# Kernel optimization log

Measured on AMD Instinct MI355X. Metric: run time of the kernel, lower is better.

The kernel has to match this reference:

```python
import jax, jax.numpy as jnp
import numpy as np

N_NODES, N_EDGES, DIM = 50000, 800000, 128


def setup_inputs() -> dict:
    key = jax.random.key(0)
    ks = jax.random.split(key, 16)
    s = 1.0 / np.sqrt(DIM)
    inp = {
        "x": jax.random.normal(ks[0], (N_NODES, DIM), dtype=jnp.float32),
        "edge_index": jax.random.randint(ks[1], (2, N_EDGES), 0, N_NODES, dtype=jnp.int64),
    }
    # 3 GIN layers, each with a 2-layer MLP (Linear-ReLU-Linear)
    for i in range(3):
        inp[f"w1_{i}"] = jax.random.normal(ks[2 + 4 * i], (DIM, DIM), dtype=jnp.float32) * s
        inp[f"b1_{i}"] = jnp.zeros((DIM,), dtype=jnp.float32)
        inp[f"w2_{i}"] = jax.random.normal(ks[3 + 4 * i], (DIM, DIM), dtype=jnp.float32) * s
        inp[f"b2_{i}"] = jnp.zeros((DIM,), dtype=jnp.float32)
    inp["wh"] = jax.random.normal(ks[14], (DIM, DIM), dtype=jnp.float32) * s
    inp["bh"] = jnp.zeros((DIM,), dtype=jnp.float32)
    return inp


def _gin_layer(h, src, dst, w1, b1, w2, b2, residual):
    # message passing: gather x[src], scatter-add at dst (aggr='sum')
    neigh = jax.ops.segment_sum(h[src], dst, num_segments=h.shape[0])
    out = h + neigh  # (1 + eps) * x + neigh, eps = 0
    out = jnp.maximum(out @ w1 + b1, 0.0) @ w2 + b2  # MLP (dropout p=0)
    if residual:  # res_fc is Identity since in_dim == out_dim
        out = out + h
    return out


def reference(x, edge_index, w1_0, b1_0, w2_0, b2_0, w1_1, b1_1, w2_1, b2_1,
              w1_2, b1_2, w2_2, b2_2, wh, bh):
    src, dst = edge_index[0], edge_index[1]
    h = x
    h = _gin_layer(h, src, dst, w1_0, b1_0, w2_0, b2_0, residual=True)
    h = _gin_layer(h, src, dst, w1_1, b1_1, w2_1, b2_1, residual=True)
    # last layer: encoding=False -> no residual
    h = _gin_layer(h, src, dst, w1_2, b1_2, w2_2, b2_2, residual=False)
    # extra_output_fc head
    return h @ wh + bh
```

## Files before the change

kernel.cpp:

```cpp
#include <hip/hip_runtime.h>
#include <hip/hip_fp16.h>

#define N_NODES 50000
#define N_EDGES 800000
#define DIM 128
#define FEAT_ELEMS (N_NODES * DIM)
#define STRIDE 64
#define NB 391
#define BCAP 3072

typedef __attribute__((ext_vector_type(8))) _Float16 f16x8;
typedef __attribute__((ext_vector_type(4))) float f32x4;
typedef __attribute__((ext_vector_type(2))) float f32x2;

#define MFMA_F16 __builtin_amdgcn_mfma_f32_16x16x32_f16


__global__ __launch_bounds__(256) void prep_combo_kernel(
    const float* __restrict__ w0, const float* __restrict__ w1,
    const float* __restrict__ w2, const float* __restrict__ w3,
    const float* __restrict__ w4, const float* __restrict__ w5,
    const float* __restrict__ w6, __half* __restrict__ dst,
    const float* __restrict__ x, __half* __restrict__ hm,
    unsigned char* __restrict__ qm, int* __restrict__ gcnt) {
    const int b = blockIdx.x;
    if (b < 112) {
        const int wsel = b >> 4;
        const int chunk = b & 15;
        const float* W;
        switch (wsel) {
            case 0: W = w0; break;
            case 1: W = w1; break;
            case 2: W = w2; break;
            case 3: W = w3; break;
            case 4: W = w4; break;
            case 5: W = w5; break;
            default: W = w6; break;
        }
        __half* d = dst + (size_t)wsel * 16384;
        int idx = chunk * 1024 + threadIdx.x;
#pragma unroll
        for (int t = 0; t < 4; ++t, idx += 256) {
            int k = idx >> 7, n = idx & 127;
            int ks = k >> 5, q = (k >> 3) & 3, j = k & 7;
            int ct = n >> 4, c = n & 15;
            int lane = q * 16 + c;
            int base = ((ks * 8 + ct) * 64 + lane) * 8 + j;
            d[base] = __float2half(W[idx]);
        }
    } else if (b < 1136) {
        int i = (b - 112) * 256 + threadIdx.x;
        const int stride = 1024 * 256;
        const int n4 = FEAT_ELEMS / 4;
        for (; i < n4; i += stride) {
            float4 v = ((const float4*)x)[i];
            __half2 h0 = __floats2half2_rn(v.x, v.y);
            __half2 h1 = __floats2half2_rn(v.z, v.w);
            uint2 u;
            u.x = *(unsigned*)&h0;
            u.y = *(unsigned*)&h1;
            ((uint2*)hm)[i] = u;
            int p = __builtin_amdgcn_cvt_pk_fp8_f32(v.x, v.y, 0, false);
            p = __builtin_amdgcn_cvt_pk_fp8_f32(v.z, v.w, p, true);
            ((int*)qm)[i] = p;
        }
    } else {
        for (int i = threadIdx.x; i < NB; i += 256) gcnt[i] = 0;
    }
}


__global__ __launch_bounds__(256) void bucket_kernel(const int* __restrict__ ei,
                                                     int* __restrict__ gcnt,
                                                     long long* __restrict__ ebuf) {
    __shared__ int hist[NB];
    __shared__ int base[NB];
    __shared__ int sh_is64;
    const int tid = threadIdx.x;
    for (int i = tid; i < NB; i += 256) hist[i] = 0;
    if (tid == 0) {
        int o = 0;
        for (int i = 1; i < 64; i += 2) o |= ei[i];
        sh_is64 = (o == 0) ? 1 : 0;
    }
    __syncthreads();
    const int e0 = blockIdx.x * 2048;
    const int is64 = sh_is64;
    int sv[8], dv[8];
    int nl = 0;
#pragma unroll
    for (int k = 0; k < 8; ++k) {
        int e = e0 + k * 256 + tid;
        if (e < N_EDGES) {
            int s = is64 ? ei[2 * e] : ei[e];
            int d = is64 ? ei[2 * (N_EDGES + e)] : ei[N_EDGES + e];
            sv[nl] = s;
            dv[nl] = d;
            atomicAdd(&hist[d >> 7], 1);
            ++nl;
        }
    }
    __syncthreads();
    for (int i = tid; i < NB; i += 256) {
        int h = hist[i];
        base[i] = h ? atomicAdd(&gcnt[i], h) : 0;
    }
    __syncthreads();
    for (int i = tid; i < NB; i += 256) hist[i] = 0;
    __syncthreads();
    for (int k = 0; k < nl; ++k) {
        int b = dv[k] >> 7;
        int r = base[b] + atomicAdd(&hist[b], 1);
        if (r < BCAP)
            ebuf[(size_t)b * BCAP + r] = ((long long)sv[k] << 32) | (unsigned)dv[k];
    }
}


__global__ __launch_bounds__(256) void build_kernel(const int* __restrict__ gcnt,
                                                    const long long* __restrict__ ebuf,
                                                    int* __restrict__ cnt,
                                                    int* __restrict__ col_idx) {
    __shared__ int cur[128];
    const int b = blockIdx.x;
    const int tid = threadIdx.x;
    if (tid < 128) cur[tid] = 0;
    __syncthreads();
    int n = gcnt[b];
    if (n > BCAP) n = BCAP;
    const long long* eb = ebuf + (size_t)b * BCAP;
    for (int i = tid; i < n; i += 256) {
        long long p = eb[i];
        int d = (int)(p & 0xFFFFFFFFll);
        int s = (int)(p >> 32);
        int slot = atomicAdd(&cur[d & 127], 1);
        if (slot < STRIDE) col_idx[d * STRIDE + slot] = s;
    }
    __syncthreads();
    int node = b * 128 + tid;
    if (tid < 128 && node < N_NODES) {
        int c = cur[tid];
        cnt[node] = (c > STRIDE) ? STRIDE : c;
    }
}


__global__ __launch_bounds__(256) void agg_kernel(const __half* __restrict__ selfH,
                                                  const unsigned char* __restrict__ Qm,
                                                  const int* __restrict__ cnt,
                                                  const int* __restrict__ col_idx,
                                                  __half* __restrict__ Tm) {
    const int hw = (blockIdx.x * 256 + threadIdx.x) >> 4;
    const int l = threadIdx.x & 15;
    const int d0 = l * 8;

    float acc[8];
    {
        uint4 sv = *(const uint4*)(selfH + (size_t)hw * DIM + d0);
        const __half2* sp = (const __half2*)&sv;
        float2 s0 = __half22float2(sp[0]), s1 = __half22float2(sp[1]);
        float2 s2 = __half22float2(sp[2]), s3 = __half22float2(sp[3]);
        acc[0] = s0.x; acc[1] = s0.y; acc[2] = s1.x; acc[3] = s1.y;
        acc[4] = s2.x; acc[5] = s2.y; acc[6] = s3.x; acc[7] = s3.y;
    }
    int d = cnt[hw];
    if (d > STRIDE) d = STRIDE;
    const int* ci = col_idx + hw * STRIDE;

#define ACCQ(U)                                                             \
    {                                                                       \
        f32x2 g0 = __builtin_amdgcn_cvt_pk_f32_fp8((int)(U).x, false);      \
        f32x2 g1 = __builtin_amdgcn_cvt_pk_f32_fp8((int)(U).x, true);       \
        f32x2 g2 = __builtin_amdgcn_cvt_pk_f32_fp8((int)(U).y, false);      \
        f32x2 g3 = __builtin_amdgcn_cvt_pk_f32_fp8((int)(U).y, true);       \
        acc[0] += g0.x; acc[1] += g0.y; acc[2] += g1.x; acc[3] += g1.y;     \
        acc[4] += g2.x; acc[5] += g2.y; acc[6] += g3.x; acc[7] += g3.y;     \
    }
    int j = 0;
    for (; j + 8 <= d; j += 8) {
        int s[8];
#pragma unroll
        for (int k = 0; k < 8; ++k) s[k] = ci[j + k];
        uint2 u[8];
#pragma unroll
        for (int k = 0; k < 8; ++k) u[k] = *(const uint2*)(Qm + (size_t)s[k] * DIM + d0);
#pragma unroll
        for (int k = 0; k < 8; ++k) ACCQ(u[k])
    }
    for (; j + 2 <= d; j += 2) {
        int s0 = ci[j], s1 = ci[j + 1];
        uint2 u0 = *(const uint2*)(Qm + (size_t)s0 * DIM + d0);
        uint2 u1 = *(const uint2*)(Qm + (size_t)s1 * DIM + d0);
        ACCQ(u0)
        ACCQ(u1)
    }
    if (j < d) {
        int s = ci[j];
        uint2 u = *(const uint2*)(Qm + (size_t)s * DIM + d0);
        ACCQ(u)
    }
#undef ACCQ

    uint4 o;
    __half2* op = (__half2*)&o;
    op[0] = __floats2half2_rn(acc[0], acc[1]);
    op[1] = __floats2half2_rn(acc[2], acc[3]);
    op[2] = __floats2half2_rn(acc[4], acc[5]);
    op[3] = __floats2half2_rn(acc[6], acc[7]);
    *(uint4*)(Tm + (size_t)hw * DIM + d0) = o;
}


template <bool RES, bool WQ>
__global__ __launch_bounds__(256, 4) void mlp_kernel(
    const __half* __restrict__ T,
    const __half* __restrict__ W1f,
    const __half* __restrict__ W2f,
    const float* __restrict__ b1,
    const float* __restrict__ b2,
    const __half* __restrict__ resH,
    __half* __restrict__ Hout,
    unsigned char* __restrict__ Qout) {
    __shared__ __align__(16) __half ul[4][2048];
    const int tid = threadIdx.x;
    const int lane = tid & 63;
    const int wid = tid >> 6;
    const int c = lane & 15;
    const int q = lane >> 4;
    const int R = (blockIdx.x * 4 + wid) * 16;
    if (R >= N_NODES) return;

    f16x8 a[4];
#pragma unroll
    for (int ks = 0; ks < 4; ++ks)
        a[ks] = *(const f16x8*)(T + (size_t)(R + c) * DIM + ks * 32 + q * 8);

    f32x4 acc1[8];
#pragma unroll
    for (int ct = 0; ct < 8; ++ct) acc1[ct] = (f32x4){0.f, 0.f, 0.f, 0.f};
#pragma unroll
    for (int ks = 0; ks < 4; ++ks) {
#pragma unroll
        for (int ct = 0; ct < 8; ++ct) {
            f16x8 b = *(const f16x8*)(W1f + (ks * 8 + ct) * 512 + lane * 8);
            acc1[ct] = MFMA_F16(a[ks], b, acc1[ct], 0, 0, 0);
        }
    }

#pragma unroll
    for (int ct = 0; ct < 8; ++ct) {
        const int col = ct * 16 + c;
        const float bv = b1[col];
#pragma unroll
        for (int rr = 0; rr < 4; ++rr) {
            const int rl = q * 4 + rr;
            ul[wid][rl * 128 + (col ^ ((rl & 7) << 3))] =
                __float2half(fmaxf(acc1[ct][rr] + bv, 0.f));
        }
    }

    f32x4 acc2[8];
#pragma unroll
    for (int ct = 0; ct < 8; ++ct) acc2[ct] = (f32x4){0.f, 0.f, 0.f, 0.f};
#pragma unroll
    for (int ks = 0; ks < 4; ++ks) {
        f16x8 ua = *(const f16x8*)&ul[wid][c * 128 + ((ks * 32 + q * 8) ^ ((c & 7) << 3))];
#pragma unroll
        for (int ct = 0; ct < 8; ++ct) {
            f16x8 b = *(const f16x8*)(W2f + (ks * 8 + ct) * 512 + lane * 8);
            acc2[ct] = MFMA_F16(ua, b, acc2[ct], 0, 0, 0);
        }
    }

#pragma unroll
    for (int ct = 0; ct < 8; ++ct) {
        const int col = ct * 16 + c;
        const float bv = b2[col];
#pragma unroll
        for (int rr = 0; rr < 4; ++rr) {
            const int rl = q * 4 + rr;
            ul[wid][rl * 128 + (col ^ (q << 4))] = __float2half(acc2[ct][rr] + bv);
        }
    }

    const int row2 = lane >> 2;
    const int cb = (lane & 3) * 8;
    const size_t grow = (size_t)(R + row2);
#pragma unroll
    for (int k = 0; k < 4; ++k) {
        const int c0 = cb + k * 32;
        uint4 hv = *(uint4*)&ul[wid][row2 * 128 + (c0 ^ ((row2 >> 2) << 4))];
        const __half2* hp = (const __half2*)&hv;
        float2 t0 = __half22float2(hp[0]), t1 = __half22float2(hp[1]);
        float2 t2 = __half22float2(hp[2]), t3 = __half22float2(hp[3]);
        float f0 = t0.x, f1 = t0.y, f2 = t1.x, f3 = t1.y;
        float f4 = t2.x, f5 = t2.y, f6 = t3.x, f7 = t3.y;
        if (RES) {
            uint4 rv = *(const uint4*)(resH + grow * DIM + c0);
            const __half2* rp = (const __half2*)&rv;
            float2 r0 = __half22float2(rp[0]), r1 = __half22float2(rp[1]);
            float2 r2 = __half22float2(rp[2]), r3 = __half22float2(rp[3]);
            f0 += r0.x; f1 += r0.y; f2 += r1.x; f3 += r1.y;
            f4 += r2.x; f5 += r2.y; f6 += r3.x; f7 += r3.y;
        }
        uint4 ov;
        __half2* op = (__half2*)&ov;
        op[0] = __floats2half2_rn(f0, f1);
        op[1] = __floats2half2_rn(f2, f3);
        op[2] = __floats2half2_rn(f4, f5);
        op[3] = __floats2half2_rn(f6, f7);
        *(uint4*)(Hout + grow * DIM + c0) = ov;
        if (WQ) {
            int q0 = __builtin_amdgcn_cvt_pk_fp8_f32(f0, f1, 0, false);
            q0 = __builtin_amdgcn_cvt_pk_fp8_f32(f2, f3, q0, true);
            int q1 = __builtin_amdgcn_cvt_pk_fp8_f32(f4, f5, 0, false);
            q1 = __builtin_amdgcn_cvt_pk_fp8_f32(f6, f7, q1, true);
            uint2 qv;
            qv.x = (unsigned)q0;
            qv.y = (unsigned)q1;
            *(uint2*)(Qout + grow * DIM + c0) = qv;
        }
    }
}


__global__ __launch_bounds__(256, 4) void gemm_head_kernel(const __half* __restrict__ T,
                                                           const __half* __restrict__ Wf,
                                                           const float* __restrict__ bias,
                                                           float* __restrict__ C) {
    const int tid = threadIdx.x;
    const int lane = tid & 63;
    const int wid = tid >> 6;
    const int c = lane & 15;
    const int q = lane >> 4;
    const int R = (blockIdx.x * 4 + wid) * 16;
    if (R >= N_NODES) return;

    f16x8 a[4];
#pragma unroll
    for (int ks = 0; ks < 4; ++ks)
        a[ks] = *(const f16x8*)(T + (size_t)(R + c) * DIM + ks * 32 + q * 8);

    f32x4 acc[8];
#pragma unroll
    for (int ct = 0; ct < 8; ++ct) acc[ct] = (f32x4){0.f, 0.f, 0.f, 0.f};
#pragma unroll
    for (int ks = 0; ks < 4; ++ks) {
#pragma unroll
        for (int ct = 0; ct < 8; ++ct) {
            f16x8 b = *(const f16x8*)(Wf + (ks * 8 + ct) * 512 + lane * 8);
            acc[ct] = MFMA_F16(a[ks], b, acc[ct], 0, 0, 0);
        }
    }

#pragma unroll
    for (int ct = 0; ct < 8; ++ct) {
        const int col = ct * 16 + c;
        const float bv = bias[col];
#pragma unroll
        for (int rr = 0; rr < 4; ++rr) {
            const int row = R + q * 4 + rr;
            C[(size_t)row * DIM + col] = acc[ct][rr] + bv;
        }
    }
}


extern "C" void kernel_launch(void* const* d_in, const int* in_sizes, int n_in,
                              void* d_out, int out_size, void* d_ws, size_t ws_size,
                              hipStream_t stream) {
    const float* x = (const float*)d_in[0];
    const int* ei = (const int*)d_in[1];
    const float* w1[3] = {(const float*)d_in[2], (const float*)d_in[6], (const float*)d_in[10]};
    const float* b1[3] = {(const float*)d_in[3], (const float*)d_in[7], (const float*)d_in[11]};
    const float* w2[3] = {(const float*)d_in[4], (const float*)d_in[8], (const float*)d_in[12]};
    const float* b2[3] = {(const float*)d_in[5], (const float*)d_in[9], (const float*)d_in[13]};
    const float* wh = (const float*)d_in[14];
    const float* bh = (const float*)d_in[15];
    float* out = (float*)d_out;

    char* ws = (char*)d_ws;
    const size_t HFEAT = (size_t)FEAT_ELEMS * sizeof(__half);
    const size_t QFEAT = (size_t)FEAT_ELEMS;
    size_t off = 0;
    int* cnt = (int*)(ws + off);                         off += 200704;
    int* col_idx = (int*)(ws + off);                     off += (size_t)N_NODES * STRIDE * 4;
    int* gcnt = (int*)(ws + off);                        off += 4096;
    __half* Wf = (__half*)(ws + off);                    off += 7 * 32768;
    long long* ebuf = (long long*)(ws + off);            off += (size_t)NB * BCAP * 8;
    __half* HMx = (__half*)(ws + off);                   off += HFEAT;
    __half* HM1 = (__half*)(ws + off);                   off += HFEAT;
    __half* HM0 = (__half*)(ws + off);                   off += HFEAT;
    __half* Tm = (__half*)(ws + off);                    off += HFEAT;
    __half* Tm3 = (__half*)(ws + off);                   off += HFEAT;
    unsigned char* Qx = (unsigned char*)(ws + off);      off += QFEAT;
    unsigned char* Q1 = (unsigned char*)(ws + off);      off += QFEAT;
    unsigned char* Q0 = (unsigned char*)(ws + off);      off += QFEAT;

    const int AGG_BLKS = N_NODES * 16 / 256;
    const int MLP_BLKS = (N_NODES / 16 + 3) / 4;

    prep_combo_kernel<<<1137, 256, 0, stream>>>(w1[0], w2[0], w1[1], w2[1], w1[2], w2[2],
                                                wh, Wf, x, HMx, Qx, gcnt);
    bucket_kernel<<<NB, 256, 0, stream>>>(ei, gcnt, ebuf);
    build_kernel<<<NB, 256, 0, stream>>>(gcnt, ebuf, cnt, col_idx);

#define WF(i) (Wf + (size_t)(i) * 16384)

    agg_kernel<<<AGG_BLKS, 256, 0, stream>>>(HMx, Qx, cnt, col_idx, Tm);
    mlp_kernel<true, true><<<MLP_BLKS, 256, 0, stream>>>(
        Tm, WF(0), WF(1), b1[0], b2[0], HMx, HM1, Q1);

    agg_kernel<<<AGG_BLKS, 256, 0, stream>>>(HM1, Q1, cnt, col_idx, Tm);
    mlp_kernel<true, true><<<MLP_BLKS, 256, 0, stream>>>(
        Tm, WF(2), WF(3), b1[1], b2[1], HM1, HM0, Q0);

    agg_kernel<<<AGG_BLKS, 256, 0, stream>>>(HM0, Q0, cnt, col_idx, Tm);
    mlp_kernel<false, false><<<MLP_BLKS, 256, 0, stream>>>(
        Tm, WF(4), WF(5), b1[2], b2[2], nullptr, Tm3, nullptr);

    gemm_head_kernel<<<MLP_BLKS, 256, 0, stream>>>(Tm3, WF(6), bh, out);
#undef WF
}
```

Measured before the change: 244.9 us.

## Fuse neighbor aggregation, MLP and output head into one GIN layer kernel

Merges the gather/aggregate kernel into the MLP kernel. Each wave aggregates its 16 rows directly into shared memory, then feeds them to the MFMA-based MLP, so the aggregate tensor no longer round-trips through global memory. The last layer also applies the head GEMM in-kernel, which drops the separate head kernel and its intermediate buffer. In exchange, the gather now runs with far fewer waves (one 16-lane group per row, 4 rows in sequence per wave), which can reduce the memory-level parallelism available to hide the irregular gather latency.

```diff
diff --git a/kernel.cpp b/kernel.cpp
--- a/kernel.cpp
+++ b/kernel.cpp
@@ -145,28 +145,32 @@
 }
 
 
-__global__ __launch_bounds__(256) void agg_kernel(const __half* __restrict__ selfH,
-                                                  const unsigned char* __restrict__ Qm,
-                                                  const int* __restrict__ cnt,
-                                                  const int* __restrict__ col_idx,
-                                                  __half* __restrict__ Tm) {
-    const int hw = (blockIdx.x * 256 + threadIdx.x) >> 4;
-    const int l = threadIdx.x & 15;
-    const int d0 = l * 8;
-
-    float acc[8];
+template <bool LAST>
+__global__ __launch_bounds__(256, 4) void gin_layer_kernel(
+    const __half* __restrict__ Hs,
+    const unsigned char* __restrict__ Qm,
+    const int* __restrict__ cnt,
+    const int* __restrict__ col_idx,
+    const __half* __restrict__ W1f,
+    const __half* __restrict__ W2f,
+    const __half* __restrict__ Whf,
+    const float* __restrict__ b1,
+    const float* __restrict__ b2,
+    const float* __restrict__ bh,
+    __half* __restrict__ Hout,
+    unsigned char* __restrict__ Qout,
+    float* __restrict__ Cout) {
+    __shared__ __align__(16) __half ul[4][2048];
+    const int tid = threadIdx.x;
+    const int lane = tid & 63;
+    const int wid = tid >> 6;
+    const int c = lane & 15;
+    const int q = lane >> 4;
+    const int R = (blockIdx.x * 4 + wid) * 16;
+    if (R >= N_NODES) return;
+
     {
-        uint4 sv = *(const uint4*)(selfH + (size_t)hw * DIM + d0);
-        const __half2* sp = (const __half2*)&sv;
-        float2 s0 = __half22float2(sp[0]), s1 = __half22float2(sp[1]);
-        float2 s2 = __half22float2(sp[2]), s3 = __half22float2(sp[3]);
-        acc[0] = s0.x; acc[1] = s0.y; acc[2] = s1.x; acc[3] = s1.y;
-        acc[4] = s2.x; acc[5] = s2.y; acc[6] = s3.x; acc[7] = s3.y;
-    }
-    int d = cnt[hw];
-    if (d > STRIDE) d = STRIDE;
-    const int* ci = col_idx + hw * STRIDE;
-
+        const int d0 = c * 8;
 #define ACCQ(U)                                                             \
     {                                                                       \
         f32x2 g0 = __builtin_amdgcn_cvt_pk_f32_fp8((int)(U).x, false);      \
@@ -176,64 +180,61 @@
         acc[0] += g0.x; acc[1] += g0.y; acc[2] += g1.x; acc[3] += g1.y;     \
         acc[4] += g2.x; acc[5] += g2.y; acc[6] += g3.x; acc[7] += g3.y;     \
     }
-    int j = 0;
-    for (; j + 8 <= d; j += 8) {
-        int s[8];
-#pragma unroll
-        for (int k = 0; k < 8; ++k) s[k] = ci[j + k];
-        uint2 u[8];
-#pragma unroll
-        for (int k = 0; k < 8; ++k) u[k] = *(const uint2*)(Qm + (size_t)s[k] * DIM + d0);
-#pragma unroll
-        for (int k = 0; k < 8; ++k) ACCQ(u[k])
-    }
-    for (; j + 2 <= d; j += 2) {
-        int s0 = ci[j], s1 = ci[j + 1];
-        uint2 u0 = *(const uint2*)(Qm + (size_t)s0 * DIM + d0);
-        uint2 u1 = *(const uint2*)(Qm + (size_t)s1 * DIM + d0);
-        ACCQ(u0)
-        ACCQ(u1)
-    }
-    if (j < d) {
-        int s = ci[j];
-        uint2 u = *(const uint2*)(Qm + (size_t)s * DIM + d0);
-        ACCQ(u)
-    }
+#pragma unroll
+        for (int it = 0; it < 4; ++it) {
+            const int rl = it * 4 + q;
+            const size_t grow = (size_t)(R + rl);
+            float acc[8];
+            {
+                uint4 sv = *(const uint4*)(Hs + grow * DIM + d0);
+                const __half2* sp = (const __half2*)&sv;
+                float2 s0 = __half22float2(sp[0]), s1 = __half22float2(sp[1]);
+                float2 s2 = __half22float2(sp[2]), s3 = __half22float2(sp[3]);
+                acc[0] = s0.x; acc[1] = s0.y; acc[2] = s1.x; acc[3] = s1.y;
+                acc[4] = s2.x; acc[5] = s2.y; acc[6] = s3.x; acc[7] = s3.y;
+            }
+            int d = cnt[grow];
+            if (d > STRIDE) d = STRIDE;
+            const int* ci = col_idx + grow * STRIDE;
+            int j = 0;
+            for (; j + 8 <= d; j += 8) {
+                int s[8];
+#pragma unroll
+                for (int k = 0; k < 8; ++k) s[k] = ci[j + k];
+                uint2 u[8];
+#pragma unroll
+                for (int k = 0; k < 8; ++k)
+                    u[k] = *(const uint2*)(Qm + (size_t)s[k] * DIM + d0);
+#pragma unroll
+                for (int k = 0; k < 8; ++k) ACCQ(u[k])
+            }
+            for (; j + 2 <= d; j += 2) {
+                int s0 = ci[j], s1 = ci[j + 1];
+                uint2 u0 = *(const uint2*)(Qm + (size_t)s0 * DIM + d0);
+                uint2 u1 = *(const uint2*)(Qm + (size_t)s1 * DIM + d0);
+                ACCQ(u0)
+                ACCQ(u1)
+            }
+            if (j < d) {
+                int s = ci[j];
+                uint2 u = *(const uint2*)(Qm + (size_t)s * DIM + d0);
+                ACCQ(u)
+            }
+            uint4 o;
+            __half2* op = (__half2*)&o;
+            op[0] = __floats2half2_rn(acc[0], acc[1]);
+            op[1] = __floats2half2_rn(acc[2], acc[3]);
+            op[2] = __floats2half2_rn(acc[4], acc[5]);
+            op[3] = __floats2half2_rn(acc[6], acc[7]);
+            *(uint4*)&ul[wid][rl * 128 + (d0 ^ ((rl & 7) << 3))] = o;
+        }
 #undef ACCQ
-
-    uint4 o;
-    __half2* op = (__half2*)&o;
-    op[0] = __floats2half2_rn(acc[0], acc[1]);
-    op[1] = __floats2half2_rn(acc[2], acc[3]);
-    op[2] = __floats2half2_rn(acc[4], acc[5]);
-    op[3] = __floats2half2_rn(acc[6], acc[7]);
-    *(uint4*)(Tm + (size_t)hw * DIM + d0) = o;
-}
-
-
-template <bool RES, bool WQ>
-__global__ __launch_bounds__(256, 4) void mlp_kernel(
-    const __half* __restrict__ T,
-    const __half* __restrict__ W1f,
-    const __half* __restrict__ W2f,
-    const float* __restrict__ b1,
-    const float* __restrict__ b2,
-    const __half* __restrict__ resH,
-    __half* __restrict__ Hout,
-    unsigned char* __restrict__ Qout) {
-    __shared__ __align__(16) __half ul[4][2048];
-    const int tid = threadIdx.x;
-    const int lane = tid & 63;
-    const int wid = tid >> 6;
-    const int c = lane & 15;
-    const int q = lane >> 4;
-    const int R = (blockIdx.x * 4 + wid) * 16;
-    if (R >= N_NODES) return;
+    }
 
     f16x8 a[4];
 #pragma unroll
     for (int ks = 0; ks < 4; ++ks)
-        a[ks] = *(const f16x8*)(T + (size_t)(R + c) * DIM + ks * 32 + q * 8);
+        a[ks] = *(const f16x8*)&ul[wid][c * 128 + ((ks * 32 + q * 8) ^ ((c & 7) << 3))];
 
     f32x4 acc1[8];
 #pragma unroll
@@ -283,34 +284,34 @@
         }
     }
 
-    const int row2 = lane >> 2;
-    const int cb = (lane & 3) * 8;
-    const size_t grow = (size_t)(R + row2);
-#pragma unroll
-    for (int k = 0; k < 4; ++k) {
-        const int c0 = cb + k * 32;
-        uint4 hv = *(uint4*)&ul[wid][row2 * 128 + (c0 ^ ((row2 >> 2) << 4))];
-        const __half2* hp = (const __half2*)&hv;
-        float2 t0 = __half22float2(hp[0]), t1 = __half22float2(hp[1]);
-        float2 t2 = __half22float2(hp[2]), t3 = __half22float2(hp[3]);
-        float f0 = t0.x, f1 = t0.y, f2 = t1.x, f3 = t1.y;
-        float f4 = t2.x, f5 = t2.y, f6 = t3.x, f7 = t3.y;
-        if (RES) {
-            uint4 rv = *(const uint4*)(resH + grow * DIM + c0);
-            const __half2* rp = (const __half2*)&rv;
-            float2 r0 = __half22float2(rp[0]), r1 = __half22float2(rp[1]);
-            float2 r2 = __half22float2(rp[2]), r3 = __half22float2(rp[3]);
-            f0 += r0.x; f1 += r0.y; f2 += r1.x; f3 += r1.y;
-            f4 += r2.x; f5 += r2.y; f6 += r3.x; f7 += r3.y;
-        }
-        uint4 ov;
-        __half2* op = (__half2*)&ov;
-        op[0] = __floats2half2_rn(f0, f1);
-        op[1] = __floats2half2_rn(f2, f3);
-        op[2] = __floats2half2_rn(f4, f5);
-        op[3] = __floats2half2_rn(f6, f7);
-        *(uint4*)(Hout + grow * DIM + c0) = ov;
-        if (WQ) {
+    if (!LAST) {
+        const int row2 = lane >> 2;
+        const int cb = (lane & 3) * 8;
+        const size_t grow = (size_t)(R + row2);
+#pragma unroll
+        for (int k = 0; k < 4; ++k) {
+            const int c0 = cb + k * 32;
+            uint4 hv = *(uint4*)&ul[wid][row2 * 128 + (c0 ^ ((row2 >> 2) << 4))];
+            const __half2* hp = (const __half2*)&hv;
+            float2 t0 = __half22float2(hp[0]), t1 = __half22float2(hp[1]);
+            float2 t2 = __half22float2(hp[2]), t3 = __half22float2(hp[3]);
+            float f0 = t0.x, f1 = t0.y, f2 = t1.x, f3 = t1.y;
+            float f4 = t2.x, f5 = t2.y, f6 = t3.x, f7 = t3.y;
+            {
+                uint4 rv = *(const uint4*)(Hs + grow * DIM + c0);
+                const __half2* rp = (const __half2*)&rv;
+                float2 r0 = __half22float2(rp[0]), r1 = __half22float2(rp[1]);
+                float2 r2 = __half22float2(rp[2]), r3 = __half22float2(rp[3]);
+                f0 += r0.x; f1 += r0.y; f2 += r1.x; f3 += r1.y;
+                f4 += r2.x; f5 += r2.y; f6 += r3.x; f7 += r3.y;
+            }
+            uint4 ov;
+            __half2* op = (__half2*)&ov;
+            op[0] = __floats2half2_rn(f0, f1);
+            op[1] = __floats2half2_rn(f2, f3);
+            op[2] = __floats2half2_rn(f4, f5);
+            op[3] = __floats2half2_rn(f6, f7);
+            *(uint4*)(Hout + grow * DIM + c0) = ov;
             int q0 = __builtin_amdgcn_cvt_pk_fp8_f32(f0, f1, 0, false);
             q0 = __builtin_amdgcn_cvt_pk_fp8_f32(f2, f3, q0, true);
             int q1 = __builtin_amdgcn_cvt_pk_fp8_f32(f4, f5, 0, false);
@@ -320,47 +321,29 @@
             qv.y = (unsigned)q1;
             *(uint2*)(Qout + grow * DIM + c0) = qv;
         }
-    }
-}
-
-
-__global__ __launch_bounds__(256, 4) void gemm_head_kernel(const __half* __restrict__ T,
-                                                           const __half* __restrict__ Wf,
-                                                           const float* __restrict__ bias,
-                                                           float* __restrict__ C) {
-    const int tid = threadIdx.x;
-    const int lane = tid & 63;
-    const int wid = tid >> 6;
-    const int c = lane & 15;
-    const int q = lane >> 4;
-    const int R = (blockIdx.x * 4 + wid) * 16;
-    if (R >= N_NODES) return;
-
-    f16x8 a[4];
-#pragma unroll
-    for (int ks = 0; ks < 4; ++ks)
-        a[ks] = *(const f16x8*)(T + (size_t)(R + c) * DIM + ks * 32 + q * 8);
-
-    f32x4 acc[8];
-#pragma unroll
-    for (int ct = 0; ct < 8; ++ct) acc[ct] = (f32x4){0.f, 0.f, 0.f, 0.f};
-#pragma unroll
-    for (int ks = 0; ks < 4; ++ks) {
+    } else {
+        f32x4 acc3[8];
+#pragma unroll
+        for (int ct = 0; ct < 8; ++ct) acc3[ct] = (f32x4){0.f, 0.f, 0.f, 0.f};
+#pragma unroll
+        for (int ks = 0; ks < 4; ++ks) {
+            f16x8 ha =
+                *(const f16x8*)&ul[wid][c * 128 + ((ks * 32 + q * 8) ^ ((c >> 2) << 4))];
+#pragma unroll
+            for (int ct = 0; ct < 8; ++ct) {
+                f16x8 b = *(const f16x8*)(Whf + (ks * 8 + ct) * 512 + lane * 8);
+                acc3[ct] = MFMA_F16(ha, b, acc3[ct], 0, 0, 0);
+            }
+        }
 #pragma unroll
         for (int ct = 0; ct < 8; ++ct) {
-            f16x8 b = *(const f16x8*)(Wf + (ks * 8 + ct) * 512 + lane * 8);
-            acc[ct] = MFMA_F16(a[ks], b, acc[ct], 0, 0, 0);
-        }
-    }
-
-#pragma unroll
-    for (int ct = 0; ct < 8; ++ct) {
-        const int col = ct * 16 + c;
-        const float bv = bias[col];
-#pragma unroll
-        for (int rr = 0; rr < 4; ++rr) {
-            const int row = R + q * 4 + rr;
-            C[(size_t)row * DIM + col] = acc[ct][rr] + bv;
+            const int col = ct * 16 + c;
+            const float bv = bh[col];
+#pragma unroll
+            for (int rr = 0; rr < 4; ++rr) {
+                const int row = R + q * 4 + rr;
+                Cout[(size_t)row * DIM + col] = acc3[ct][rr] + bv;
+            }
         }
     }
 }
@@ -391,14 +374,11 @@
     __half* HMx = (__half*)(ws + off);                   off += HFEAT;
     __half* HM1 = (__half*)(ws + off);                   off += HFEAT;
     __half* HM0 = (__half*)(ws + off);                   off += HFEAT;
-    __half* Tm = (__half*)(ws + off);                    off += HFEAT;
-    __half* Tm3 = (__half*)(ws + off);                   off += HFEAT;
     unsigned char* Qx = (unsigned char*)(ws + off);      off += QFEAT;
     unsigned char* Q1 = (unsigned char*)(ws + off);      off += QFEAT;
     unsigned char* Q0 = (unsigned char*)(ws + off);      off += QFEAT;
 
-    const int AGG_BLKS = N_NODES * 16 / 256;
-    const int MLP_BLKS = (N_NODES / 16 + 3) / 4;
+    const int GIN_BLKS = (N_NODES / 16 + 3) / 4;
 
     prep_combo_kernel<<<1137, 256, 0, stream>>>(w1[0], w2[0], w1[1], w2[1], w1[2], w2[2],
                                                 wh, Wf, x, HMx, Qx, gcnt);
@@ -407,18 +387,16 @@
 
 #define WF(i) (Wf + (size_t)(i) * 16384)
 
-    agg_kernel<<<AGG_BLKS, 256, 0, stream>>>(HMx, Qx, cnt, col_idx, Tm);
-    mlp_kernel<true, true><<<MLP_BLKS, 256, 0, stream>>>(
-        Tm, WF(0), WF(1), b1[0], b2[0], HMx, HM1, Q1);
-
-    agg_kernel<<<AGG_BLKS, 256, 0, stream>>>(HM1, Q1, cnt, col_idx, Tm);
-    mlp_kernel<true, true><<<MLP_BLKS, 256, 0, stream>>>(
-        Tm, WF(2), WF(3), b1[1], b2[1], HM1, HM0, Q0);
-
-    agg_kernel<<<AGG_BLKS, 256, 0, stream>>>(HM0, Q0, cnt, col_idx, Tm);
-    mlp_kernel<false, false><<<MLP_BLKS, 256, 0, stream>>>(
-        Tm, WF(4), WF(5), b1[2], b2[2], nullptr, Tm3, nullptr);
-
-    gemm_head_kernel<<<MLP_BLKS, 256, 0, stream>>>(Tm3, WF(6), bh, out);
+    gin_layer_kernel<false><<<GIN_BLKS, 256, 0, stream>>>(
+        HMx, Qx, cnt, col_idx, WF(0), WF(1), nullptr, b1[0], b2[0], nullptr,
+        HM1, Q1, nullptr);
+
+    gin_layer_kernel<false><<<GIN_BLKS, 256, 0, stream>>>(
+        HM1, Q1, cnt, col_idx, WF(2), WF(3), nullptr, b1[1], b2[1], nullptr,
+        HM0, Q0, nullptr);
+
+    gin_layer_kernel<true><<<GIN_BLKS, 256, 0, stream>>>(
+        HM0, Q0, cnt, col_idx, WF(4), WF(5), WF(6), b1[2], b2[2], bh,
+        nullptr, nullptr, out);
 #undef WF
 }
```

New measurement: 237.1 us, median of 2. 1.03x faster.
